# Optimization experiments

Measured on AMD Instinct MI355X. Metric: run time of the kernel, lower is better.

Reference implementation:

```python
import jax, jax.numpy as jnp
import numpy as np

D = 512        # model dim
NH = 8         # heads
NL = 4         # layers
MSL = 2048     # max_seq_len for relative positional bias
ITEM_V, CATE_V, SEG_V = 100000, 1000, 2
EPS = 1e-5


def layer_norm(x, w, b):
    mu = jnp.mean(x, axis=-1, keepdims=True)
    var = jnp.mean((x - mu) ** 2, axis=-1, keepdims=True)
    return (x - mu) * jax.lax.rsqrt(var + EPS) * w + b


def setup_inputs() -> dict:
    key = jax.random.key(0)
    ks = jax.random.split(key, 16)
    B, L = 8, 1023
    inp = {
        'historical_item_ids': jax.random.randint(ks[0], (B, L), 0, ITEM_V, dtype=jnp.int32),
        'historical_cate_ids': jax.random.randint(ks[1], (B, L), 0, CATE_V, dtype=jnp.int32),
        'historical_len': jax.random.randint(ks[2], (B,), 0, L, dtype=jnp.int32),
        'target_item_id': jax.random.randint(ks[3], (B,), 0, ITEM_V, dtype=jnp.int32),
        'target_cate_id': jax.random.randint(ks[4], (B,), 0, CATE_V, dtype=jnp.int32),
        # embeddings (init std 0.02 like _init_weights)
        'item_emb': 0.02 * jax.random.normal(ks[5], (ITEM_V, D), jnp.float32),
        'cate_emb': 0.02 * jax.random.normal(ks[6], (CATE_V, D), jnp.float32),
        'seg_emb': 0.02 * jax.random.normal(ks[7], (SEG_V, D), jnp.float32),
        # per-layer stacked params
        'W1': 0.02 * jax.random.normal(ks[8], (NL, D, 4 * D), jnp.float32),
        'b1': jnp.zeros((NL, 4 * D), jnp.float32),
        'W2': 0.02 * jax.random.normal(ks[9], (NL, D, D), jnp.float32),
        'b2': jnp.zeros((NL, D), jnp.float32),
        'ln1_w': jnp.ones((NL, D), jnp.float32), 'ln1_b': jnp.zeros((NL, D), jnp.float32),
        'ln2_w': jnp.ones((NL, D), jnp.float32), 'ln2_b': jnp.zeros((NL, D), jnp.float32),
        'pos_w': 0.02 * jax.random.normal(ks[10], (NL, 2 * MSL - 1), jnp.float32),
        'lnf_w': jnp.ones((D,), jnp.float32), 'lnf_b': jnp.zeros((D,), jnp.float32),
    }
    return inp


def _forward(historical_item_ids, historical_cate_ids, historical_len,
             target_item_id, target_cate_id,
             item_emb, cate_emb, seg_emb, W1, b1, W2, b2,
             ln1_w, ln1_b, ln2_w, ln2_b, pos_w, lnf_w, lnf_b):
    B = historical_item_ids.shape[0]
    ar = jnp.arange(B)
    pad = jnp.zeros((B, 1), historical_item_ids.dtype)
    ids = jnp.concatenate([historical_item_ids, pad], axis=1).at[ar, historical_len].set(target_item_id)
    cids = jnp.concatenate([historical_cate_ids, pad], axis=1).at[ar, historical_len].set(target_cate_id)
    S = ids.shape[1]
    seg = jnp.zeros_like(ids).at[ar, historical_len].set(1)

    h = item_emb[ids] + cate_emb[cids] + seg_emb[seg]  # [B,S,D]

    # relative position bias indices: bias[i,j] = pos_w[MSL-1 + j - i]
    rel_idx = MSL - 1 + jnp.arange(S)[None, :] - jnp.arange(S)[:, None]  # [S,S]
    causal = jnp.tril(jnp.ones((S, S), h.dtype))  # multiplicative mask (mask >= 0)

    for l in range(NL):
        z = jax.nn.silu(h @ W1[l] + b1[l])  # [B,S,4D]
        u, q, k, v = jnp.split(z, 4, axis=-1)
        resh = lambda t: t.reshape(B, S, NH, D // NH).transpose(0, 2, 1, 3)  # [B,H,S,hd]
        u, q, k, v = resh(u), resh(q), resh(k), resh(v)
        bias = pos_w[l][rel_idx]  # [S,S]
        att = jax.nn.silu(jnp.einsum('bhsd,bhtd->bhst', q, k) + bias) * causal
        y = jnp.einsum('bhst,bhtd->bhsd', att, v) * u
        y = y.transpose(0, 2, 1, 3).reshape(B, S, D)
        y = layer_norm(y, ln1_w[l], ln1_b[l])
        y = y @ W2[l] + b2[l]
        h = layer_norm(y + h, ln2_w[l], ln2_b[l])  # dropout p=0 (eval)

    return layer_norm(h, lnf_w, lnf_b)


def reference(historical_item_ids, historical_cate_ids, historical_len,
              target_item_id, target_cate_id,
              item_emb, cate_emb, seg_emb, W1, b1, W2, b2,
              ln1_w, ln1_b, ln2_w, ln2_b, pos_w, lnf_w, lnf_b):
    return _forward(historical_item_ids, historical_cate_ids, historical_len,
                    target_item_id, target_cate_id,
                    item_emb, cate_emb, seg_emb, W1, b1, W2, b2,
                    ln1_w, ln1_b, ln2_w, ln2_b, pos_w, lnf_w, lnf_b)
```

## Files before the change

### kernel.cpp

```cpp
#include <hip/hip_runtime.h>
#include <cstddef>


#define D_MODEL 512
#define S_LEN 1024
#define NHEADS 8

typedef __bf16 bf16x8 __attribute__((ext_vector_type(8)));
typedef float f32x4 __attribute__((ext_vector_type(4)));
typedef unsigned short us4 __attribute__((ext_vector_type(4)));
typedef unsigned short us8 __attribute__((ext_vector_type(8)));

__device__ __forceinline__ float silu_f(float x) {
  return x / (1.f + __expf(-x));
}
__device__ __forceinline__ unsigned short f2bf(float f) {
  unsigned int u = __float_as_uint(f);
  u += 0x7FFF + ((u >> 16) & 1);
  return (unsigned short)(u >> 16);
}
__device__ __forceinline__ float bf2f(unsigned short s) {
  return __uint_as_float(((unsigned int)s) << 16);
}
__device__ __forceinline__ void gll16(const void* g, void* l) {
  __builtin_amdgcn_global_load_lds(
      (const __attribute__((address_space(1))) unsigned int*)g,
      (__attribute__((address_space(3))) unsigned int*)l, 16, 0, 0);
}

__global__ __launch_bounds__(256) void embed_kernel(
    const int* __restrict__ hist_i, const int* __restrict__ hist_c,
    const int* __restrict__ hlen, const int* __restrict__ tgt_i,
    const int* __restrict__ tgt_c, const float* __restrict__ item_emb,
    const float* __restrict__ cate_emb, const float* __restrict__ seg_emb,
    float* __restrict__ h32, unsigned short* __restrict__ hbf) {
  int bs = blockIdx.x;
  int b = bs >> 10, s = bs & 1023;
  int l = hlen[b];
  int id, cid, sg;
  if (s == l)       { id = tgt_i[b]; cid = tgt_c[b]; sg = 1; }
  else if (s < 1023){ id = hist_i[b * 1023 + s]; cid = hist_c[b * 1023 + s]; sg = 0; }
  else              { id = 0; cid = 0; sg = 0; }
  const float* ie = item_emb + (size_t)id * D_MODEL;
  const float* ce = cate_emb + (size_t)cid * D_MODEL;
  const float* se = seg_emb + (size_t)sg * D_MODEL;
  float* hr = h32 + (size_t)bs * D_MODEL;
  unsigned short* hb = hbf + (size_t)bs * D_MODEL;
  for (int d = threadIdx.x; d < D_MODEL; d += 256) {
    float v = ie[d] + ce[d] + se[d];
    hr[d] = v;
    hb[d] = f2bf(v);
  }
}

__global__ __launch_bounds__(256) void transpose_kernel(
    const float* __restrict__ W, unsigned short* __restrict__ Wt,
    int K, int N) {
  const int l = blockIdx.z;
  W += (size_t)l * K * N;
  Wt += (size_t)l * K * N;
  const int n0 = blockIdx.x * 64, k0 = blockIdx.y * 64;
  __shared__ float T[64][65];
  const int tid = threadIdx.x;
  const int rr = tid >> 4, cc = (tid & 15) * 4;
#pragma unroll
  for (int p = 0; p < 4; p++) {
    const int r = rr + p * 16;
    const float4 v = *reinterpret_cast<const float4*>(&W[(size_t)(k0 + r) * N + n0 + cc]);
    T[r][cc] = v.x; T[r][cc + 1] = v.y; T[r][cc + 2] = v.z; T[r][cc + 3] = v.w;
  }
  __syncthreads();
#pragma unroll
  for (int p = 0; p < 4; p++) {
    const int r = rr + p * 16;
    us4 o = { f2bf(T[cc + 0][r]), f2bf(T[cc + 1][r]),
              f2bf(T[cc + 2][r]), f2bf(T[cc + 3][r]) };
    *reinterpret_cast<us4*>(&Wt[(size_t)(n0 + r) * K + k0 + cc]) = o;
  }
}

template <int TM, int TN, int SWZ, int EPI_SILU, typename OutT>
__global__ __launch_bounds__(256) void mfma_gemm(
    const unsigned short* __restrict__ A, const unsigned short* __restrict__ Bt,
    const float* __restrict__ bias, OutT* __restrict__ C,
    int M, int N, int K) {
  constexpr int MI = TM / 32, NI = TN / 32;
  __shared__ unsigned short As[TM * 64];
  __shared__ unsigned short Bs[TN * 64];
  const int tid = threadIdx.x;
  const int w = tid >> 6, lane = tid & 63, lm = lane & 15, quad = lane >> 4;
  const int wm = w & 1, wn = w >> 1;
  int m0, n0;
  if (SWZ) {
    const int id = blockIdx.x;
    const int xcd = id & 7, j = id >> 3;
    const int mPerX = (M / TM) >> 3;
    m0 = (xcd * mPerX + (j % mPerX)) * TM;
    n0 = (j / mPerX) * TN;
  } else {
    m0 = blockIdx.y * TM;
    n0 = blockIdx.x * TN;
  }

  f32x4 acc[MI][NI] = {};

  for (int k0 = 0; k0 < K; k0 += 64) {
#pragma unroll
    for (int p = 0; p < TM / 32; p++) {
      const int g = p * 256 + tid;
      const int r = g >> 3;
      const int lc = (g & 7) ^ (r & 7);
      gll16(A + (size_t)(m0 + r) * K + k0 + lc * 8, &As[g * 8]);
    }
#pragma unroll
    for (int p = 0; p < TN / 32; p++) {
      const int g = p * 256 + tid;
      const int r = g >> 3;
      const int lc = (g & 7) ^ (r & 7);
      gll16(Bt + (size_t)(n0 + r) * K + k0 + lc * 8, &Bs[g * 8]);
    }
    __syncthreads();
#pragma unroll
    for (int ki = 0; ki < 2; ki++) {
      bf16x8 af[MI], bfr[NI];
#pragma unroll
      for (int mi = 0; mi < MI; mi++) {
        const int r = wm * (TM / 2) + mi * 16 + lm;
        const int p = (ki * 4 + quad) ^ (lm & 7);
        af[mi] = *reinterpret_cast<const bf16x8*>(&As[r * 64 + p * 8]);
      }
#pragma unroll
      for (int ni = 0; ni < NI; ni++) {
        const int r = wn * (TN / 2) + ni * 16 + lm;
        const int p = (ki * 4 + quad) ^ (lm & 7);
        bfr[ni] = *reinterpret_cast<const bf16x8*>(&Bs[r * 64 + p * 8]);
      }
#pragma unroll
      for (int mi = 0; mi < MI; mi++)
#pragma unroll
        for (int ni = 0; ni < NI; ni++)
          acc[mi][ni] = __builtin_amdgcn_mfma_f32_16x16x32_bf16(
              af[mi], bfr[ni], acc[mi][ni], 0, 0, 0);
    }
    __syncthreads();
  }

#pragma unroll
  for (int ni = 0; ni < NI; ni++) {
    const int n = n0 + wn * (TN / 2) + ni * 16 + lm;
    const float bv = bias[n];
#pragma unroll
    for (int mi = 0; mi < MI; mi++) {
      const int mbase = m0 + wm * (TM / 2) + mi * 16 + quad * 4;
#pragma unroll
      for (int reg = 0; reg < 4; reg++) {
        float v = acc[mi][ni][reg] + bv;
        if (EPI_SILU) v = silu_f(v);
        if constexpr (sizeof(OutT) == 2)
          C[(size_t)(mbase + reg) * N + n] = f2bf(v);
        else
          C[(size_t)(mbase + reg) * N + n] = v;
      }
    }
  }
}

#define LDR 72
__global__ __launch_bounds__(256) void attn_kernel(
    const unsigned short* __restrict__ z, const float* __restrict__ posw,
    unsigned short* __restrict__ y) {
  const int hh = blockIdx.y, b = blockIdx.z;
  __shared__ alignas(16) unsigned short Ks[64 * LDR];
  __shared__ alignas(16) unsigned short Vt[64 * LDR];
  __shared__ alignas(16) unsigned short Ps[64 * LDR];
  __shared__ float bias_s[128];
  const unsigned short* zb = z + (size_t)b * S_LEN * 2048;
  const int tid = threadIdx.x;
  const int w = tid >> 6, lane = tid & 63, lm = lane & 15, quad = lane >> 4;

#pragma unroll
  for (int phase = 0; phase < 2; phase++) {
    const int qt = phase == 0 ? (int)blockIdx.x : 15 - (int)blockIdx.x;
    const int s0 = qt * 64;
    const int srow = s0 + w * 16 + lm;

    const bf16x8 qb0 = *reinterpret_cast<const bf16x8*>(
        zb + (size_t)srow * 2048 + 512 + hh * 64 + quad * 8);
    const bf16x8 qb1 = *reinterpret_cast<const bf16x8*>(
        zb + (size_t)srow * 2048 + 512 + hh * 64 + 32 + quad * 8);

    f32x4 O[4] = {};

    for (int kt = 0; kt <= qt; kt++) {
      const int t0 = kt * 64;
      __syncthreads();
#pragma unroll
      for (int p = 0; p < 2; p++) {
        const int g = p * 256 + tid;
        const int r = g >> 3, ch = (g & 7) * 8;
        *reinterpret_cast<us8*>(&Ks[r * LDR + ch]) =
            *reinterpret_cast<const us8*>(zb + (size_t)(t0 + r) * 2048 + 1024 + hh * 64 + ch);
      }
      {
        const int t = (tid >> 4) * 4;
        const int d = (tid & 15) * 4;
        unsigned short c[4][4];
#pragma unroll
        for (int r = 0; r < 4; r++) {
          const us4 v = *reinterpret_cast<const us4*>(
              zb + (size_t)(t0 + t + r) * 2048 + 1536 + hh * 64 + d);
          c[r][0] = v.x; c[r][1] = v.y; c[r][2] = v.z; c[r][3] = v.w;
        }
        const int tb = t >> 3, ti = t & 7;
#pragma unroll
        for (int j = 0; j < 4; j++) {
          const int dd = d + j;
          us4 o = { c[0][j], c[1][j], c[2][j], c[3][j] };
          *reinterpret_cast<us4*>(&Vt[dd * LDR + ((tb ^ (dd & 7)) << 3) + ti]) = o;
        }
      }
      if (tid < 128) bias_s[tid] = posw[2047 + t0 - s0 - 63 + tid];
      __syncthreads();

#pragma unroll
      for (int tt = 0; tt < 4; tt++) {
        const bf16x8 ka0 = *reinterpret_cast<const bf16x8*>(&Ks[(tt * 16 + lm) * LDR + quad * 8]);
        const bf16x8 ka1 = *reinterpret_cast<const bf16x8*>(&Ks[(tt * 16 + lm) * LDR + 32 + quad * 8]);
        f32x4 st = {};
        st = __builtin_amdgcn_mfma_f32_16x16x32_bf16(ka0, qb0, st, 0, 0, 0);
        st = __builtin_amdgcn_mfma_f32_16x16x32_bf16(ka1, qb1, st, 0, 0, 0);
        const int bbase = 63 + tt * 16 + quad * 4 - w * 16 - lm;
        const int tq = t0 + tt * 16 + quad * 4;
        us4 pv;
        unsigned short* pp = (unsigned short*)&pv;
#pragma unroll
        for (int i = 0; i < 4; i++) {
          const float x = st[i] + bias_s[bbase + i];
          const float val = (tq + i <= srow) ? silu_f(x) : 0.f;
          pp[i] = f2bf(val);
        }
        *reinterpret_cast<us4*>(&Ps[(w * 16 + lm) * LDR + tt * 16 + quad * 4]) = pv;
      }

      const bf16x8 pa0 = *reinterpret_cast<const bf16x8*>(&Ps[(w * 16 + lm) * LDR + quad * 8]);
      const bf16x8 pa1 = *reinterpret_cast<const bf16x8*>(&Ps[(w * 16 + lm) * LDR + 32 + quad * 8]);
#pragma unroll
      for (int ct = 0; ct < 4; ct++) {
        const int d = ct * 16 + lm;
        const bf16x8 vb0 = *reinterpret_cast<const bf16x8*>(
            &Vt[d * LDR + ((quad ^ (d & 7)) << 3)]);
        const bf16x8 vb1 = *reinterpret_cast<const bf16x8*>(
            &Vt[d * LDR + (((4 + quad) ^ (d & 7)) << 3)]);
        O[ct] = __builtin_amdgcn_mfma_f32_16x16x32_bf16(pa0, vb0, O[ct], 0, 0, 0);
        O[ct] = __builtin_amdgcn_mfma_f32_16x16x32_bf16(pa1, vb1, O[ct], 0, 0, 0);
      }
    }

    {
      const int sbase = s0 + w * 16 + quad * 4;
#pragma unroll
      for (int ct = 0; ct < 4; ct++) {
        const int d = ct * 16 + lm;
#pragma unroll
        for (int i = 0; i < 4; i++) {
          const int sg = sbase + i;
          const float u = bf2f(zb[(size_t)sg * 2048 + hh * 64 + d]);
          y[((size_t)(b * S_LEN + sg)) * D_MODEL + hh * 64 + d] = f2bf(O[ct][i] * u);
        }
      }
    }
  }
}

template <typename XT>
__global__ __launch_bounds__(256) void ln_kernel(
    const XT* __restrict__ x, const float* __restrict__ res,
    const float* __restrict__ w, const float* __restrict__ bb,
    float* __restrict__ o32, unsigned short* __restrict__ obf) {
  const int wv = threadIdx.x >> 6, lane = threadIdx.x & 63;
  const size_t row = blockIdx.x * 4 + wv;
  const int c0 = lane * 8;
  float v[8];
  if constexpr (sizeof(XT) == 2) {
    const us8 u = *reinterpret_cast<const us8*>(&x[row * D_MODEL + c0]);
#pragma unroll
    for (int i = 0; i < 8; i++) v[i] = bf2f(u[i]);
  } else {
    const float4 a = *reinterpret_cast<const float4*>(&x[row * D_MODEL + c0]);
    const float4 c = *reinterpret_cast<const float4*>(&x[row * D_MODEL + c0 + 4]);
    v[0] = a.x; v[1] = a.y; v[2] = a.z; v[3] = a.w;
    v[4] = c.x; v[5] = c.y; v[6] = c.z; v[7] = c.w;
  }
  if (res) {
    const float4 r0 = *reinterpret_cast<const float4*>(&res[row * D_MODEL + c0]);
    const float4 r1 = *reinterpret_cast<const float4*>(&res[row * D_MODEL + c0 + 4]);
    v[0] += r0.x; v[1] += r0.y; v[2] += r0.z; v[3] += r0.w;
    v[4] += r1.x; v[5] += r1.y; v[6] += r1.z; v[7] += r1.w;
  }
  float s = 0.f, ss = 0.f;
#pragma unroll
  for (int i = 0; i < 8; i++) { s += v[i]; ss += v[i] * v[i]; }
#pragma unroll
  for (int off = 32; off; off >>= 1) {
    s += __shfl_down(s, off, 64);
    ss += __shfl_down(ss, off, 64);
  }
  s = __shfl(s, 0, 64);
  ss = __shfl(ss, 0, 64);
  const float mu = s * (1.f / D_MODEL);
  const float rstd = rsqrtf(ss * (1.f / D_MODEL) - mu * mu + 1e-5f);
  const float4 w0 = *reinterpret_cast<const float4*>(&w[c0]);
  const float4 w1 = *reinterpret_cast<const float4*>(&w[c0 + 4]);
  const float4 b0 = *reinterpret_cast<const float4*>(&bb[c0]);
  const float4 b1 = *reinterpret_cast<const float4*>(&bb[c0 + 4]);
  float r[8];
  r[0] = (v[0] - mu) * rstd * w0.x + b0.x;
  r[1] = (v[1] - mu) * rstd * w0.y + b0.y;
  r[2] = (v[2] - mu) * rstd * w0.z + b0.z;
  r[3] = (v[3] - mu) * rstd * w0.w + b0.w;
  r[4] = (v[4] - mu) * rstd * w1.x + b1.x;
  r[5] = (v[5] - mu) * rstd * w1.y + b1.y;
  r[6] = (v[6] - mu) * rstd * w1.z + b1.z;
  r[7] = (v[7] - mu) * rstd * w1.w + b1.w;
  if (o32) {
    *reinterpret_cast<float4*>(&o32[row * D_MODEL + c0]) = make_float4(r[0], r[1], r[2], r[3]);
    *reinterpret_cast<float4*>(&o32[row * D_MODEL + c0 + 4]) = make_float4(r[4], r[5], r[6], r[7]);
  }
  if (obf) {
    us8 q = { f2bf(r[0]), f2bf(r[1]), f2bf(r[2]), f2bf(r[3]),
              f2bf(r[4]), f2bf(r[5]), f2bf(r[6]), f2bf(r[7]) };
    *reinterpret_cast<us8*>(&obf[row * D_MODEL + c0]) = q;
  }
}

extern "C" void kernel_launch(void* const* d_in, const int* in_sizes, int n_in,
                              void* d_out, int out_size, void* d_ws, size_t ws_size,
                              hipStream_t stream) {
  const int* hist_i = (const int*)d_in[0];
  const int* hist_c = (const int*)d_in[1];
  const int* hlen   = (const int*)d_in[2];
  const int* tgt_i  = (const int*)d_in[3];
  const int* tgt_c  = (const int*)d_in[4];
  const float* item_emb = (const float*)d_in[5];
  const float* cate_emb = (const float*)d_in[6];
  const float* seg_emb  = (const float*)d_in[7];
  const float* W1   = (const float*)d_in[8];
  const float* b1   = (const float*)d_in[9];
  const float* W2   = (const float*)d_in[10];
  const float* b2   = (const float*)d_in[11];
  const float* ln1w = (const float*)d_in[12];
  const float* ln1b = (const float*)d_in[13];
  const float* ln2w = (const float*)d_in[14];
  const float* ln2b = (const float*)d_in[15];
  const float* posw = (const float*)d_in[16];
  const float* lnfw = (const float*)d_in[17];
  const float* lnfb = (const float*)d_in[18];
  float* out = (float*)d_out;

  char* ws = (char*)d_ws;
  float*          h32 = (float*)(ws);
  unsigned short* hbf = (unsigned short*)(ws + (16u << 20));
  unsigned short* zbf = (unsigned short*)(ws + (24u << 20));
  unsigned short* ybf = (unsigned short*)(ws + (56u << 20));
  unsigned short* yab = (unsigned short*)(ws + (64u << 20));
  unsigned short* tbf = yab;
  unsigned short* W1t = (unsigned short*)(ws + (80u << 20));
  unsigned short* W2t = (unsigned short*)(ws + (88u << 20));

  const int ROWS = 8 * S_LEN;

  transpose_kernel<<<dim3(2048 / 64, 512 / 64, 4), 256, 0, stream>>>(W1, W1t, 512, 2048);
  transpose_kernel<<<dim3(512 / 64, 512 / 64, 4), 256, 0, stream>>>(W2, W2t, 512, 512);
  embed_kernel<<<ROWS, 256, 0, stream>>>(hist_i, hist_c, hlen, tgt_i, tgt_c,
                                         item_emb, cate_emb, seg_emb, h32, hbf);
  for (int l = 0; l < 4; l++) {
    mfma_gemm<256, 128, 1, 1, unsigned short><<<512, 256, 0, stream>>>(
        hbf, W1t + (size_t)l * 2048 * 512, b1 + (size_t)l * 2048, zbf, ROWS, 2048, 512);
    attn_kernel<<<dim3(8, NHEADS, 8), 256, 0, stream>>>(
        zbf, posw + (size_t)l * 4095, yab);
    ln_kernel<unsigned short><<<ROWS / 4, 256, 0, stream>>>(
        yab, nullptr, ln1w + l * 512, ln1b + l * 512, nullptr, ybf);
    mfma_gemm<64, 128, 0, 0, unsigned short><<<dim3(512 / 128, ROWS / 64), 256, 0, stream>>>(
        ybf, W2t + (size_t)l * 512 * 512, b2 + (size_t)l * 512, tbf, ROWS, 512, 512);
    ln_kernel<unsigned short><<<ROWS / 4, 256, 0, stream>>>(
        tbf, h32, ln2w + l * 512, ln2b + l * 512, h32, hbf);
  }
  ln_kernel<float><<<ROWS / 4, 256, 0, stream>>>(h32, nullptr, lnfw, lnfb, out, nullptr);
}
```

Before: 805.5 us.

## Double-buffer K/V tiles in attention with register prefetch and MFMA priority

The attention kernel now prefetches the next K/V/bias tile from global memory into registers while computing on the current tile. The tile is then written into one of two shared-memory buffers, which removes one barrier per iteration. s_setprio is also raised around the MFMA instructions to favour matrix issue across waves. In exchange it uses more LDS and more registers, which may reduce occupancy.

New measurement: 797.7 us. No clear change (-1.0%).

```diff
diff --git a/kernel.cpp b/kernel.cpp
--- a/kernel.cpp
+++ b/kernel.cpp
@@ -170,13 +170,18 @@
     const unsigned short* __restrict__ z, const float* __restrict__ posw,
     unsigned short* __restrict__ y) {
   const int hh = blockIdx.y, b = blockIdx.z;
-  __shared__ alignas(16) unsigned short Ks[64 * LDR];
-  __shared__ alignas(16) unsigned short Vt[64 * LDR];
+  __shared__ alignas(16) unsigned short Ks[2 * 64 * LDR];
+  __shared__ alignas(16) unsigned short Vt[2 * 64 * LDR];
   __shared__ alignas(16) unsigned short Ps[64 * LDR];
-  __shared__ float bias_s[128];
+  __shared__ float bias_s[2][128];
   const unsigned short* zb = z + (size_t)b * S_LEN * 2048;
   const int tid = threadIdx.x;
   const int w = tid >> 6, lane = tid & 63, lm = lane & 15, quad = lane >> 4;
+
+  const int kr0r = tid >> 3, kr0c = (tid & 7) * 8;
+  const int kr1r = (256 + tid) >> 3, kr1c = (tid & 7) * 8;
+  const int vt = (tid >> 4) * 4, vd = (tid & 15) * 4;
+  const int vtb = vt >> 3, vti = vt & 7;
 
 #pragma unroll
   for (int phase = 0; phase < 2; phase++) {
@@ -191,68 +196,98 @@
 
     f32x4 O[4] = {};
 
+    us8 kr0, kr1;
+    us4 vr0, vr1, vr2, vr3;
+    float br = 0.f;
+
+    auto load_stage = [&](int kt) {
+      const int t0 = kt * 64;
+      kr0 = *reinterpret_cast<const us8*>(
+          zb + (size_t)(t0 + kr0r) * 2048 + 1024 + hh * 64 + kr0c);
+      kr1 = *reinterpret_cast<const us8*>(
+          zb + (size_t)(t0 + kr1r) * 2048 + 1024 + hh * 64 + kr1c);
+      vr0 = *reinterpret_cast<const us4*>(
+          zb + (size_t)(t0 + vt + 0) * 2048 + 1536 + hh * 64 + vd);
+      vr1 = *reinterpret_cast<const us4*>(
+          zb + (size_t)(t0 + vt + 1) * 2048 + 1536 + hh * 64 + vd);
+      vr2 = *reinterpret_cast<const us4*>(
+          zb + (size_t)(t0 + vt + 2) * 2048 + 1536 + hh * 64 + vd);
+      vr3 = *reinterpret_cast<const us4*>(
+          zb + (size_t)(t0 + vt + 3) * 2048 + 1536 + hh * 64 + vd);
+      if (tid < 128) br = posw[2047 + t0 - s0 - 63 + tid];
+    };
+
+    auto write_stage = [&](int cur) {
+      unsigned short* KsC = Ks + cur * (64 * LDR);
+      unsigned short* VtC = Vt + cur * (64 * LDR);
+      *reinterpret_cast<us8*>(&KsC[kr0r * LDR + kr0c]) = kr0;
+      *reinterpret_cast<us8*>(&KsC[kr1r * LDR + kr1c]) = kr1;
+      unsigned short c[4][4];
+      c[0][0] = vr0.x; c[0][1] = vr0.y; c[0][2] = vr0.z; c[0][3] = vr0.w;
+      c[1][0] = vr1.x; c[1][1] = vr1.y; c[1][2] = vr1.z; c[1][3] = vr1.w;
+      c[2][0] = vr2.x; c[2][1] = vr2.y; c[2][2] = vr2.z; c[2][3] = vr2.w;
+      c[3][0] = vr3.x; c[3][1] = vr3.y; c[3][2] = vr3.z; c[3][3] = vr3.w;
+#pragma unroll
+      for (int j = 0; j < 4; j++) {
+        const int dd = vd + j;
+        us4 o = { c[0][j], c[1][j], c[2][j], c[3][j] };
+        *reinterpret_cast<us4*>(&VtC[dd * LDR + ((vtb ^ (dd & 7)) << 3) + vti]) = o;
+      }
+      if (tid < 128) bias_s[cur][tid] = br;
+    };
+
+    load_stage(0);
+    __syncthreads();
+
     for (int kt = 0; kt <= qt; kt++) {
+      const int cur = kt & 1;
+      write_stage(cur);
+      __syncthreads();
+      if (kt < qt) load_stage(kt + 1);
+
+      const unsigned short* KsC = Ks + cur * (64 * LDR);
+      const unsigned short* VtC = Vt + cur * (64 * LDR);
       const int t0 = kt * 64;
-      __syncthreads();
-#pragma unroll
-      for (int p = 0; p < 2; p++) {
-        const int g = p * 256 + tid;
-        const int r = g >> 3, ch = (g & 7) * 8;
-        *reinterpret_cast<us8*>(&Ks[r * LDR + ch]) =
-            *reinterpret_cast<const us8*>(zb + (size_t)(t0 + r) * 2048 + 1024 + hh * 64 + ch);
-      }
-      {
-        const int t = (tid >> 4) * 4;
-        const int d = (tid & 15) * 4;
-        unsigned short c[4][4];
-#pragma unroll
-        for (int r = 0; r < 4; r++) {
-          const us4 v = *reinterpret_cast<const us4*>(
-              zb + (size_t)(t0 + t + r) * 2048 + 1536 + hh * 64 + d);
-          c[r][0] = v.x; c[r][1] = v.y; c[r][2] = v.z; c[r][3] = v.w;
-        }
-        const int tb = t >> 3, ti = t & 7;
-#pragma unroll
-        for (int j = 0; j < 4; j++) {
-          const int dd = d + j;
-          us4 o = { c[0][j], c[1][j], c[2][j], c[3][j] };
-          *reinterpret_cast<us4*>(&Vt[dd * LDR + ((tb ^ (dd & 7)) << 3) + ti]) = o;
-        }
-      }
-      if (tid < 128) bias_s[tid] = posw[2047 + t0 - s0 - 63 + tid];
-      __syncthreads();
 
 #pragma unroll
       for (int tt = 0; tt < 4; tt++) {
-        const bf16x8 ka0 = *reinterpret_cast<const bf16x8*>(&Ks[(tt * 16 + lm) * LDR + quad * 8]);
-        const bf16x8 ka1 = *reinterpret_cast<const bf16x8*>(&Ks[(tt * 16 + lm) * LDR + 32 + quad * 8]);
+        const bf16x8 ka0 = *reinterpret_cast<const bf16x8*>(
+            &KsC[(tt * 16 + lm) * LDR + quad * 8]);
+        const bf16x8 ka1 = *reinterpret_cast<const bf16x8*>(
+            &KsC[(tt * 16 + lm) * LDR + 32 + quad * 8]);
         f32x4 st = {};
+        __builtin_amdgcn_s_setprio(1);
         st = __builtin_amdgcn_mfma_f32_16x16x32_bf16(ka0, qb0, st, 0, 0, 0);
         st = __builtin_amdgcn_mfma_f32_16x16x32_bf16(ka1, qb1, st, 0, 0, 0);
+        __builtin_amdgcn_s_setprio(0);
         const int bbase = 63 + tt * 16 + quad * 4 - w * 16 - lm;
         const int tq = t0 + tt * 16 + quad * 4;
         us4 pv;
         unsigned short* pp = (unsigned short*)&pv;
 #pragma unroll
         for (int i = 0; i < 4; i++) {
-          const float x = st[i] + bias_s[bbase + i];
+          const float x = st[i] + bias_s[cur][bbase + i];
           const float val = (tq + i <= srow) ? silu_f(x) : 0.f;
           pp[i] = f2bf(val);
         }
         *reinterpret_cast<us4*>(&Ps[(w * 16 + lm) * LDR + tt * 16 + quad * 4]) = pv;
       }
 
-      const bf16x8 pa0 = *reinterpret_cast<const bf16x8*>(&Ps[(w * 16 + lm) * LDR + quad * 8]);
-      const bf16x8 pa1 = *reinterpret_cast<const bf16x8*>(&Ps[(w * 16 + lm) * LDR + 32 + quad * 8]);
+      const bf16x8 pa0 = *reinterpret_cast<const bf16x8*>(
+          &Ps[(w * 16 + lm) * LDR + quad * 8]);
+      const bf16x8 pa1 = *reinterpret_cast<const bf16x8*>(
+          &Ps[(w * 16 + lm) * LDR + 32 + quad * 8]);
 #pragma unroll
       for (int ct = 0; ct < 4; ct++) {
         const int d = ct * 16 + lm;
         const bf16x8 vb0 = *reinterpret_cast<const bf16x8*>(
-            &Vt[d * LDR + ((quad ^ (d & 7)) << 3)]);
+            &VtC[d * LDR + ((quad ^ (d & 7)) << 3)]);
         const bf16x8 vb1 = *reinterpret_cast<const bf16x8*>(
-            &Vt[d * LDR + (((4 + quad) ^ (d & 7)) << 3)]);
+            &VtC[d * LDR + (((4 + quad) ^ (d & 7)) << 3)]);
+        __builtin_amdgcn_s_setprio(1);
         O[ct] = __builtin_amdgcn_mfma_f32_16x16x32_bf16(pa0, vb0, O[ct], 0, 0, 0);
         O[ct] = __builtin_amdgcn_mfma_f32_16x16x32_bf16(pa1, vb1, O[ct], 0, 0, 0);
+        __builtin_amdgcn_s_setprio(0);
       }
     }
 
```
